# Kernel tuning notes

Hardware: AMD Instinct MI355X
Metric: run time of the kernel (lower is better)

## Reference

```python
import jax, jax.numpy as jnp
import numpy as np

N_NODES = 100000


def setup_inputs() -> dict:
    key = jax.random.key(0)
    ks = jax.random.split(key, 9)
    E = 1600000
    x = jax.random.normal(ks[0], (N_NODES, 12), dtype=jnp.float32)
    edge_index = jax.random.randint(ks[1], (2, E), 0, N_NODES, dtype=jnp.int64)
    def glorot(k, shape):
        lim = float(np.sqrt(6.0 / (shape[0] + shape[1])))
        return jax.random.uniform(k, shape, jnp.float32, -lim, lim)
    return {
        "x": x,
        "edge_index": edge_index,
        "W1": glorot(ks[2], (12, 64)),
        "b1": jnp.zeros((64,), jnp.float32),
        "W2": glorot(ks[3], (64, 128)),
        "b2": jnp.zeros((128,), jnp.float32),
        "W3": glorot(ks[4], (128, 96)),
        "b3": jnp.zeros((96,), jnp.float32),
    }


def reference(x, edge_index, W1, b1, W2, b2, W3, b3):
    N = x.shape[0]
    F_channel, n_his = 8, 12
    src, dst = edge_index[0], edge_index[1]
    # add self loops (PyG GCNConv default)
    loop = jnp.arange(N, dtype=src.dtype)
    src = jnp.concatenate([src, loop])
    dst = jnp.concatenate([dst, loop])
    # symmetric normalization: norm_e = deg[src]^-1/2 * deg[dst]^-1/2
    deg = jax.ops.segment_sum(jnp.ones_like(src, dtype=x.dtype), dst, num_segments=N)
    dinv = jnp.where(deg > 0, jax.lax.rsqrt(deg), 0.0)
    norm = dinv[src] * dinv[dst]  # [E+N]

    def gcn(h, W, b):
        hw = h @ W  # transform first (out_ch <= in-edge fanout cost)
        agg = jax.ops.segment_sum(hw[src] * norm[:, None], dst, num_segments=N)
        return agg + b

    h = jax.nn.relu(gcn(x, W1, b1))
    h = jax.nn.relu(gcn(h, W2, b2))
    h = gcn(h, W3, b3)
    return h.reshape(N, F_channel, n_his)
```

## Files before the change

kernel.cpp:

```cpp
#include <hip/hip_runtime.h>
#include <hip/hip_bf16.h>
#include <hip/hip_fp16.h>


static inline int cdiv(int a, int b) { return (a + b - 1) / b; }
constexpr int BLOCK = 256;
constexpr int BSHIFT = 9;
constexpr int BNODES = 1 << BSHIFT;

typedef float nfloat4 __attribute__((ext_vector_type(4)));
typedef _Float16 f16x8 __attribute__((ext_vector_type(8)));
typedef float f32x16 __attribute__((ext_vector_type(16)));


__device__ __forceinline__ void nt_store_raw16(void* p, float4 v) {
    nfloat4 nv;
    nv.x = v.x; nv.y = v.y; nv.z = v.z; nv.w = v.w;
    __builtin_nontemporal_store(nv, (nfloat4*)p);
}

struct h4 { __half2 a, b; };
__device__ __forceinline__ void store_h4(__half* p, float4 v) {
    h4 r;
    r.a = __floats2half2_rn(v.x, v.y);
    r.b = __floats2half2_rn(v.z, v.w);
    *(h4*)p = r;
}

__device__ __forceinline__ void h8_add(float* acc, float4 raw) {
    union { float4 f; __half2 h[4]; } u;
    u.f = raw;
#pragma unroll
    for (int j = 0; j < 4; ++j) {
        float2 p = __half22float2(u.h[j]);
        acc[2 * j] += p.x;
        acc[2 * j + 1] += p.y;
    }
}


template <int CHUNK>
__global__ void bucket_count_kernel(const int* __restrict__ dst, int E,
                                    int* __restrict__ bcnt, int NB) {
    __shared__ int cnt[256];
    for (int i = threadIdx.x; i < NB; i += blockDim.x) cnt[i] = 0;
    __syncthreads();
    const int e0 = blockIdx.x * CHUNK;
    const int e1 = min(e0 + CHUNK, E);
    for (int e = e0 + threadIdx.x; e < e1; e += blockDim.x)
        atomicAdd(&cnt[dst[e] >> BSHIFT], 1);
    __syncthreads();
    for (int i = threadIdx.x; i < NB; i += blockDim.x)
        if (cnt[i]) atomicAdd(&bcnt[i], cnt[i]);
}

__global__ void bucket_scan_kernel(const int* __restrict__ bcnt, int* __restrict__ gbase,
                                   int* __restrict__ gcur, int NB) {
    __shared__ int tmp[256];
    int t = threadIdx.x;
    int v = (t < NB) ? bcnt[t] : 0;
    tmp[t] = v;
    __syncthreads();
    for (int off = 1; off < 256; off <<= 1) {
        int add = (t >= off) ? tmp[t - off] : 0;
        __syncthreads();
        tmp[t] += add;
        __syncthreads();
    }
    if (t < NB) { int ex = tmp[t] - v; gbase[t] = ex; gcur[t] = ex; }
}

template <int CHUNK>
__global__ void bin_edges_kernel(const int* __restrict__ ei, int E,
                                 int* __restrict__ gcur, unsigned* __restrict__ binned,
                                 int NB) {
    __shared__ int cnt[256], base[256], rk[256];
    for (int i = threadIdx.x; i < NB; i += blockDim.x) { cnt[i] = 0; rk[i] = 0; }
    __syncthreads();
    const int e0 = blockIdx.x * CHUNK;
    const int e1 = min(e0 + CHUNK, E);
    for (int e = e0 + threadIdx.x; e < e1; e += blockDim.x)
        atomicAdd(&cnt[ei[E + e] >> BSHIFT], 1);
    __syncthreads();
    for (int i = threadIdx.x; i < NB; i += blockDim.x)
        base[i] = atomicAdd(&gcur[i], cnt[i]);
    __syncthreads();
    for (int e = e0 + threadIdx.x; e < e1; e += blockDim.x) {
        int s = ei[e], d = ei[E + e];
        int b = d >> BSHIFT;
        int r = atomicAdd(&rk[b], 1);
        binned[base[b] + r] = (unsigned)s | ((unsigned)(d & (BNODES - 1)) << 17);
    }
}

__global__ void csr_fill_kernel(const int* __restrict__ gbase, const int* __restrict__ bcnt,
                                const unsigned* __restrict__ binned,
                                int* __restrict__ deg, float* __restrict__ dinv,
                                int* __restrict__ row_ptr, int* __restrict__ csr_src,
                                int* __restrict__ dh, int N) {
    __shared__ int c[BNODES];
    __shared__ int ps[256];
    __shared__ int dhloc[64];
    const int t = threadIdx.x;
    const int b = blockIdx.x;
    const int node0 = b << BSHIFT;
    if (t < BNODES) c[t] = 0;
    if (t < 64) dhloc[t] = 0;
    __syncthreads();
    const int base = gbase[b];
    const int end = base + bcnt[b];
    for (int e = base + t; e < end; e += 1024)
        atomicAdd(&c[binned[e] >> 17], 1);
    __syncthreads();
    int s0 = 0, s1 = 0;
    if (t < 256) {
        s0 = c[2 * t]; s1 = c[2 * t + 1];
        ps[t] = s0 + s1;
    }
    __syncthreads();
    for (int off = 1; off < 256; off <<= 1) {
        int add = (t >= off && t < 256) ? ps[t - off] : 0;
        __syncthreads();
        if (t < 256) ps[t] += add;
        __syncthreads();
    }
    if (t < 256) {
        const int ex = ps[t] - (s0 + s1);
        const int p0 = base + ex;
        const int p1 = p0 + s0;
        const int n0 = node0 + 2 * t;
        if (n0 < N) {
            row_ptr[n0] = p0; deg[n0] = s0; dinv[n0] = rsqrtf((float)s0 + 1.0f);
            atomicAdd(&dhloc[min(s0, 63)], 1);
            if (n0 + 1 < N) {
                row_ptr[n0 + 1] = p1; deg[n0 + 1] = s1; dinv[n0 + 1] = rsqrtf((float)s1 + 1.0f);
                atomicAdd(&dhloc[min(s1, 63)], 1);
            }
        }
        c[2 * t] = p0; c[2 * t + 1] = p1;
    }
    __syncthreads();
    if (t < 64 && dhloc[t]) atomicAdd(&dh[t], dhloc[t]);
    for (int e = base + t; e < end; e += 1024) {
        unsigned sd = binned[e];
        int pos = atomicAdd(&c[sd >> 17], 1);
        csr_src[pos] = (int)(sd & 0x1FFFFu);
    }
}


__global__ void dscan_kernel(int* __restrict__ dh) {
    __shared__ int tmp[64];
    int t = threadIdx.x;
    int v = dh[t];
    tmp[t] = v;
    __syncthreads();
    for (int off = 1; off < 64; off <<= 1) {
        int add = (t >= off) ? tmp[t - off] : 0;
        __syncthreads();
        tmp[t] += add;
        __syncthreads();
    }
    dh[t] = tmp[t] - v;
}

__global__ void dperm_kernel(const int* __restrict__ deg, const int* __restrict__ row_ptr,
                             const float* __restrict__ dinv, int* __restrict__ dh,
                             int4* __restrict__ hdr, int N) {
    __shared__ int cnt[64], base[64], rk[64];
    const int t = threadIdx.x;
    if (t < 64) { cnt[t] = 0; rk[t] = 0; }
    __syncthreads();
    const int i = blockIdx.x * blockDim.x + t;
    const int d = (i < N) ? deg[i] : 0;
    const int myb = (i < N) ? min(d, 63) : -1;
    if (myb >= 0) atomicAdd(&cnt[myb], 1);
    __syncthreads();
    if (t < 64) base[t] = cnt[t] ? atomicAdd(&dh[t], cnt[t]) : 0;
    __syncthreads();
    if (myb >= 0) {
        int r = atomicAdd(&rk[myb], 1);
        int slot = base[myb] + r;
        int4 h;
        h.x = row_ptr[i];
        h.y = d;
        h.z = i;
        h.w = __float_as_int(dinv[i]);
        hdr[N - 1 - slot] = h;
    }
}


__global__ void prescale_h_kernel(const float* __restrict__ x, const float* __restrict__ dinv,
                                  __half* __restrict__ xs, int N) {
    int i = blockIdx.x * blockDim.x + threadIdx.x;
    if (i >= N) return;
    float di = dinv[i];
    const float4* xr = (const float4*)(x + (size_t)i * 12);
    float4 a = xr[0], b = xr[1], c = xr[2];
    union { float4 f; __half2 h[4]; } u0, u1;
    u0.h[0] = __floats2half2_rn(a.x * di, a.y * di);
    u0.h[1] = __floats2half2_rn(a.z * di, a.w * di);
    u0.h[2] = __floats2half2_rn(b.x * di, b.y * di);
    u0.h[3] = __floats2half2_rn(b.z * di, b.w * di);
    u1.h[0] = __floats2half2_rn(c.x * di, c.y * di);
    u1.h[1] = __floats2half2_rn(c.z * di, c.w * di);
    u1.h[2] = __floats2half2_rn(0.f, 0.f);
    u1.h[3] = __floats2half2_rn(0.f, 0.f);
    float4* op = (float4*)(xs + (size_t)i * 16);
    op[0] = u0.f;
    op[1] = u1.f;
}


__global__ void gather_x_t1_kernel(const int4* __restrict__ hdr,
                                   const int* __restrict__ csr_src,
                                   const __half* __restrict__ xs,
                                   const float* __restrict__ W1,
                                   const float* __restrict__ b1,
                                   __half* __restrict__ h1h, int N) {
    __shared__ float W1s[12 * 64];
    __shared__ float xrow[128][12];
    const int tid = threadIdx.x;
    for (int u = tid; u < 12 * 64 / 4; u += 256)
        ((float4*)W1s)[u] = ((const float4*)W1)[u];

    const int t = blockIdx.x * 256 + tid;
    const bool valid = (t < N * 2);
    const int slot = t >> 1;
    const int c = t & 1;
    const int nl = tid >> 1;
    int4 H = valid ? hdr[slot] : make_int4(0, 0, 0, 0);
    const int* __restrict__ sp = csr_src + H.x;
    const int n = valid ? H.y : 0;
    const int i = H.z;
    const float di = __int_as_float(H.w);
    const int f0 = c * 8;

    float acc[8];
    {
        union { float4 f; __half2 h[4]; } u;
        u.f = *(const float4*)(xs + (size_t)i * 16 + f0);
#pragma unroll
        for (int j = 0; j < 4; ++j) {
            float2 p = __half22float2(u.h[j]);
            acc[2 * j] = p.x; acc[2 * j + 1] = p.y;
        }
    }

    int k = 0;
    if (n >= 8) {
        int s[8];
#pragma unroll
        for (int j = 0; j < 8; ++j) s[j] = sp[j];
        for (; k + 16 <= n; k += 8) {
            int ns[8];
#pragma unroll
            for (int j = 0; j < 8; ++j) ns[j] = sp[k + 8 + j];
            float4 v[8];
#pragma unroll
            for (int j = 0; j < 8; ++j) v[j] = *(const float4*)(xs + (size_t)s[j] * 16 + f0);
#pragma unroll
            for (int j = 0; j < 8; ++j) h8_add(acc, v[j]);
#pragma unroll
            for (int j = 0; j < 8; ++j) s[j] = ns[j];
        }
        float4 v[8];
#pragma unroll
        for (int j = 0; j < 8; ++j) v[j] = *(const float4*)(xs + (size_t)s[j] * 16 + f0);
#pragma unroll
        for (int j = 0; j < 8; ++j) h8_add(acc, v[j]);
        k += 8;
    }
    for (; k + 4 <= n; k += 4) {
        int s0 = sp[k + 0], s1 = sp[k + 1], s2 = sp[k + 2], s3 = sp[k + 3];
        float4 v0 = *(const float4*)(xs + (size_t)s0 * 16 + f0);
        float4 v1 = *(const float4*)(xs + (size_t)s1 * 16 + f0);
        float4 v2 = *(const float4*)(xs + (size_t)s2 * 16 + f0);
        float4 v3 = *(const float4*)(xs + (size_t)s3 * 16 + f0);
        h8_add(acc, v0); h8_add(acc, v1); h8_add(acc, v2); h8_add(acc, v3);
    }
    for (; k < n; ++k) {
        float4 v = *(const float4*)(xs + (size_t)sp[k] * 16 + f0);
        h8_add(acc, v);
    }

    if (valid) {
        if (c == 0) {
#pragma unroll
            for (int j = 0; j < 8; ++j) xrow[nl][j] = acc[j] * di;
        } else {
#pragma unroll
            for (int j = 0; j < 4; ++j) xrow[nl][8 + j] = acc[j] * di;
        }
    }
    __syncthreads();
    if (!valid) return;

    float xr[12];
#pragma unroll
    for (int j = 0; j < 12; ++j) xr[j] = xrow[nl][j];

    __half* op = h1h + (size_t)i * 64 + c * 32;
#pragma unroll
    for (int g = 0; g < 8; ++g) {
        const int c0 = c * 32 + g * 4;
        float4 r = *(const float4*)(b1 + c0);
#pragma unroll
        for (int kk = 0; kk < 12; ++kk) {
            const float4 w = *(const float4*)(W1s + kk * 64 + c0);
            r.x = fmaf(xr[kk], w.x, r.x);
            r.y = fmaf(xr[kk], w.y, r.y);
            r.z = fmaf(xr[kk], w.z, r.z);
            r.w = fmaf(xr[kk], w.w, r.w);
        }
        r.x = fmaxf(r.x, 0.f) * di; r.y = fmaxf(r.y, 0.f) * di;
        r.z = fmaxf(r.z, 0.f) * di; r.w = fmaxf(r.w, 0.f) * di;
        store_h4(op + g * 4, r);
    }
}


__global__ void prep_w_kernel(const float* __restrict__ W2, const float* __restrict__ W3,
                              __half* __restrict__ W2T, __half* __restrict__ W3T) {
    int i = blockIdx.x * 256 + threadIdx.x;
    if (i < 64 * 128) {
        int k = i >> 7, n = i & 127;
        W2T[n * 64 + k] = __float2half(W2[i]);
    } else {
        int j = i - 64 * 128;
        if (j < 128 * 96) {
            int k = j / 96, n = j - k * 96;
            W3T[n * 128 + k] = __float2half(W3[j]);
        }
    }
}

__global__ void __launch_bounds__(256, 2)
fused_g64_t2t3_kernel(const __half* __restrict__ h1h,
                      const int* __restrict__ row_ptr, const int* __restrict__ deg,
                      const int* __restrict__ csr_src, const float* __restrict__ dinv,
                      const __half* __restrict__ W2T,
                      const float* __restrict__ b2,
                      const __half* __restrict__ W3T,
                      __half* __restrict__ out,
                      int N) {
    constexpr int LDH = 136;
    __shared__ _Float16 buf[4][32 * LDH];
    const int tid = threadIdx.x;
    const int lane = tid & 63;
    const int wid = tid >> 6;
    const int l31 = lane & 31;
    const int lh = lane >> 5;
    const int NT = N >> 5;
    const int t0 = blockIdx.x * 4;

    {
        const int nr = tid >> 3;
        const int f0 = (tid & 7) * 8;
#pragma unroll 1
        for (int p = 0; p < 4; ++p) {
            const int t = t0 + p;
            if (t >= NT) break;
            const int i = (t << 5) + nr;
            const int* __restrict__ sp = csr_src + row_ptr[i];
            const int n = deg[i];
            const float di = dinv[i];

            float acc[8];
            {
                union { float4 f; __half2 h[4]; } u;
                u.f = *(const float4*)(h1h + (size_t)i * 64 + f0);
#pragma unroll
                for (int j = 0; j < 4; ++j) {
                    float2 pp = __half22float2(u.h[j]);
                    acc[2 * j] = pp.x; acc[2 * j + 1] = pp.y;
                }
            }

            int k = 0;
            if (n >= 8) {
                int s[8];
#pragma unroll
                for (int j = 0; j < 8; ++j) s[j] = sp[j];
                for (; k + 16 <= n; k += 8) {
                    int ns[8];
#pragma unroll
                    for (int j = 0; j < 8; ++j) ns[j] = sp[k + 8 + j];
                    float4 v[8];
#pragma unroll
                    for (int j = 0; j < 8; ++j) v[j] = *(const float4*)(h1h + (size_t)s[j] * 64 + f0);
#pragma unroll
                    for (int j = 0; j < 8; ++j) h8_add(acc, v[j]);
#pragma unroll
                    for (int j = 0; j < 8; ++j) s[j] = ns[j];
                }
                float4 v[8];
#pragma unroll
                for (int j = 0; j < 8; ++j) v[j] = *(const float4*)(h1h + (size_t)s[j] * 64 + f0);
#pragma unroll
                for (int j = 0; j < 8; ++j) h8_add(acc, v[j]);
                k += 8;
            }
            for (; k + 4 <= n; k += 4) {
                int s0 = sp[k + 0], s1 = sp[k + 1], s2 = sp[k + 2], s3 = sp[k + 3];
                float4 v0 = *(const float4*)(h1h + (size_t)s0 * 64 + f0);
                float4 v1 = *(const float4*)(h1h + (size_t)s1 * 64 + f0);
                float4 v2 = *(const float4*)(h1h + (size_t)s2 * 64 + f0);
                float4 v3 = *(const float4*)(h1h + (size_t)s3 * 64 + f0);
                h8_add(acc, v0); h8_add(acc, v1); h8_add(acc, v2); h8_add(acc, v3);
            }
            for (; k < n; ++k) {
                float4 v = *(const float4*)(h1h + (size_t)sp[k] * 64 + f0);
                h8_add(acc, v);
            }

            union { float4 f; __half2 h[4]; } o;
            o.h[0] = __floats2half2_rn(acc[0] * di, acc[1] * di);
            o.h[1] = __floats2half2_rn(acc[2] * di, acc[3] * di);
            o.h[2] = __floats2half2_rn(acc[4] * di, acc[5] * di);
            o.h[3] = __floats2half2_rn(acc[6] * di, acc[7] * di);
            *(float4*)(&buf[p][nr * LDH + f0]) = o.f;
        }
    }
    __syncthreads();

    const int t = t0 + wid;
    if (t >= NT) return;
    const int r0 = t << 5;
    _Float16* hs = buf[wid];

    float b2v[4];
#pragma unroll
    for (int nt = 0; nt < 4; ++nt) b2v[nt] = b2[nt * 32 + l31];

    f16x8 a2[4];
#pragma unroll
    for (int kb = 0; kb < 4; ++kb)
        a2[kb] = *(const f16x8*)(hs + l31 * LDH + kb * 16 + lh * 8);

#pragma unroll
    for (int nt = 0; nt < 4; ++nt) {
        f32x16 c = {0.f, 0.f, 0.f, 0.f, 0.f, 0.f, 0.f, 0.f,
                    0.f, 0.f, 0.f, 0.f, 0.f, 0.f, 0.f, 0.f};
#pragma unroll
        for (int kb = 0; kb < 4; ++kb) {
            f16x8 b = *(const f16x8*)(W2T + (size_t)(nt * 32 + l31) * 64 + kb * 16 + lh * 8);
            c = __builtin_amdgcn_mfma_f32_32x32x16_f16(a2[kb], b, c, 0, 0, 0);
        }
#pragma unroll
        for (int r = 0; r < 16; ++r) {
            int row = (r & 3) + 8 * (r >> 2) + 4 * lh;
            float v = fmaxf(c[r] + b2v[nt], 0.f);
            hs[row * LDH + nt * 32 + l31] = (_Float16)v;
        }
    }

    f16x8 a3[8];
#pragma unroll
    for (int kb = 0; kb < 8; ++kb)
        a3[kb] = *(const f16x8*)(hs + l31 * LDH + kb * 16 + lh * 8);
    float4 dv[4];
#pragma unroll
    for (int rg = 0; rg < 4; ++rg)
        dv[rg] = *(const float4*)(dinv + r0 + rg * 8 + lh * 4);
#pragma unroll
    for (int nt = 0; nt < 3; ++nt) {
        f32x16 c = {0.f, 0.f, 0.f, 0.f, 0.f, 0.f, 0.f, 0.f,
                    0.f, 0.f, 0.f, 0.f, 0.f, 0.f, 0.f, 0.f};
#pragma unroll
        for (int kb = 0; kb < 8; ++kb) {
            f16x8 b = *(const f16x8*)(W3T + (size_t)(nt * 32 + l31) * 128 + kb * 16 + lh * 8);
            c = __builtin_amdgcn_mfma_f32_32x32x16_f16(a3[kb], b, c, 0, 0, 0);
        }
#pragma unroll
        for (int r = 0; r < 16; ++r) {
            int row = (r & 3) + 8 * (r >> 2) + 4 * lh;
            float dvv = ((const float*)&dv[r >> 2])[r & 3];
            hs[row * LDH + nt * 32 + l31] = (_Float16)(c[r] * dvv);
        }
    }

#pragma unroll
    for (int it = 0; it < 6; ++it) {
        int id = lane + it * 64;
        int row = id / 12, ch = id - row * 12;
        float4 v = *(const float4*)(hs + row * LDH + ch * 8);
        *(float4*)((char*)(out + (size_t)r0 * 96) + (size_t)id * 16) = v;
    }
}


template <int F, bool HAS_BIAS, bool OUT_HALF>
__global__ void gather_h_kernel(const int4* __restrict__ hdr, const int* __restrict__ csr_src,
                                const __half* __restrict__ hws,
                                const float* __restrict__ b, void* __restrict__ out_v, int N) {
    constexpr int TPN = F / 8;
    int t = blockIdx.x * blockDim.x + threadIdx.x;
    if (t >= N * TPN) return;
    int slot = t / TPN;
    int c = t - slot * TPN;
    const int4 H = hdr[slot];
    const int* __restrict__ sp = csr_src + H.x;
    const int n = H.y;
    const int i = H.z;
    const float di = __int_as_float(H.w);
    int f0 = c * 8;

    float acc[8];
    {
        union { float4 f; __half2 h[4]; } u;
        u.f = *(const float4*)(hws + (size_t)i * F + f0);
#pragma unroll
        for (int j = 0; j < 4; ++j) {
            float2 p = __half22float2(u.h[j]);
            acc[2 * j] = p.x; acc[2 * j + 1] = p.y;
        }
    }

    int k = 0;
    if (n >= 8) {
        int s[8];
#pragma unroll
        for (int j = 0; j < 8; ++j) s[j] = sp[j];
        for (; k + 16 <= n; k += 8) {
            int ns[8];
#pragma unroll
            for (int j = 0; j < 8; ++j) ns[j] = sp[k + 8 + j];
            float4 v[8];
#pragma unroll
            for (int j = 0; j < 8; ++j) v[j] = *(const float4*)(hws + (size_t)s[j] * F + f0);
#pragma unroll
            for (int j = 0; j < 8; ++j) h8_add(acc, v[j]);
#pragma unroll
            for (int j = 0; j < 8; ++j) s[j] = ns[j];
        }
        float4 v[8];
#pragma unroll
        for (int j = 0; j < 8; ++j) v[j] = *(const float4*)(hws + (size_t)s[j] * F + f0);
#pragma unroll
        for (int j = 0; j < 8; ++j) h8_add(acc, v[j]);
        k += 8;
    }
    for (; k + 4 <= n; k += 4) {
        int s0 = sp[k + 0], s1 = sp[k + 1], s2 = sp[k + 2], s3 = sp[k + 3];
        float4 v0 = *(const float4*)(hws + (size_t)s0 * F + f0);
        float4 v1 = *(const float4*)(hws + (size_t)s1 * F + f0);
        float4 v2 = *(const float4*)(hws + (size_t)s2 * F + f0);
        float4 v3 = *(const float4*)(hws + (size_t)s3 * F + f0);
        h8_add(acc, v0); h8_add(acc, v1); h8_add(acc, v2); h8_add(acc, v3);
    }
    for (; k < n; ++k) {
        float4 v = *(const float4*)(hws + (size_t)sp[k] * F + f0);
        h8_add(acc, v);
    }

    float4 r0, r1;
    if (HAS_BIAS) {
        const float4 bb0 = *(const float4*)(b + f0);
        const float4 bb1 = *(const float4*)(b + f0 + 4);
        r0.x = fmaf(acc[0], di, bb0.x); r0.y = fmaf(acc[1], di, bb0.y);
        r0.z = fmaf(acc[2], di, bb0.z); r0.w = fmaf(acc[3], di, bb0.w);
        r1.x = fmaf(acc[4], di, bb1.x); r1.y = fmaf(acc[5], di, bb1.y);
        r1.z = fmaf(acc[6], di, bb1.z); r1.w = fmaf(acc[7], di, bb1.w);
    } else {
        r0.x = acc[0] * di; r0.y = acc[1] * di; r0.z = acc[2] * di; r0.w = acc[3] * di;
        r1.x = acc[4] * di; r1.y = acc[5] * di; r1.z = acc[6] * di; r1.w = acc[7] * di;
    }
    if (OUT_HALF) {
        union { float4 f; __half2 h[4]; } u;
        u.h[0] = __floats2half2_rn(r0.x, r0.y);
        u.h[1] = __floats2half2_rn(r0.z, r0.w);
        u.h[2] = __floats2half2_rn(r1.x, r1.y);
        u.h[3] = __floats2half2_rn(r1.z, r1.w);
        nt_store_raw16((__half*)out_v + (size_t)i * F + f0, u.f);
    } else {
        float* op = (float*)out_v + (size_t)i * F + f0;
        nt_store_raw16(op, r0);
        nt_store_raw16(op + 4, r1);
    }
}


extern "C" void kernel_launch(void* const* d_in, const int* in_sizes, int n_in,
                              void* d_out, int out_size, void* d_ws, size_t ws_size,
                              hipStream_t stream) {
    const float* x  = (const float*)d_in[0];
    const int*   ei = (const int*)d_in[1];
    const float* W1 = (const float*)d_in[2];
    const float* b1 = (const float*)d_in[3];
    const float* W2 = (const float*)d_in[4];
    const float* b2 = (const float*)d_in[5];
    const float* W3 = (const float*)d_in[6];
    const float* b3 = (const float*)d_in[7];
    float* out = (float*)d_out;

    const int N = in_sizes[0] / 12;
    const int E = in_sizes[1] / 2;
    const int NB = cdiv(N, BNODES);

    char* ws = (char*)d_ws;
    int*   deg     = (int*)ws;    ws += (size_t)N * sizeof(int);
    int*   row_ptr = (int*)ws;    ws += (size_t)N * sizeof(int);
    int*   bcnt    = (int*)ws;    ws += 256 * sizeof(int);
    int*   dh      = (int*)ws;    ws += 64 * sizeof(int);
    int*   gbase   = (int*)ws;    ws += 256 * sizeof(int);
    int*   gcur    = (int*)ws;    ws += 256 * sizeof(int);
    float* dinv    = (float*)ws;  ws += (size_t)N * sizeof(float);
    int4*  hdr     = (int4*)ws;   ws += (size_t)N * sizeof(int4);
    __half* W2Th   = (__half*)ws; ws += 128 * 64 * sizeof(__half);
    __half* W3Th   = (__half*)ws; ws += 96 * 128 * sizeof(__half);
    int*   csr_src = (int*)ws;    ws += (size_t)E * sizeof(int);
    float* bufA    = (float*)ws;  ws += (size_t)N * 128 * sizeof(float);
    float* bufB    = (float*)ws;
    unsigned* binned = (unsigned*)bufB;

    hipMemsetAsync(bcnt, 0, (256 + 64) * sizeof(int), stream);
    prep_w_kernel<<<80, 256, 0, stream>>>(W2, W3, W2Th, W3Th);
    bucket_count_kernel<8192><<<cdiv(E, 8192), BLOCK, 0, stream>>>(ei + E, E, bcnt, NB);
    bucket_scan_kernel<<<1, 256, 0, stream>>>(bcnt, gbase, gcur, NB);
    bin_edges_kernel<8192><<<cdiv(E, 8192), BLOCK, 0, stream>>>(ei, E, gcur, binned, NB);
    csr_fill_kernel<<<NB, 1024, 0, stream>>>(gbase, bcnt, binned, deg, dinv, row_ptr,
                                             csr_src, dh, N);

    dscan_kernel<<<1, 64, 0, stream>>>(dh);
    dperm_kernel<<<cdiv(N, BLOCK), BLOCK, 0, stream>>>(deg, row_ptr, dinv, dh, hdr, N);

    prescale_h_kernel<<<cdiv(N, BLOCK), BLOCK, 0, stream>>>(x, dinv, (__half*)bufA, N);
    gather_x_t1_kernel<<<cdiv(N * 2, BLOCK), BLOCK, 0, stream>>>(
        hdr, csr_src, (const __half*)bufA, W1, b1, (__half*)bufB, N);

    fused_g64_t2t3_kernel<<<cdiv(N / 32, 4), 256, 0, stream>>>(
        (const __half*)bufB, row_ptr, deg, csr_src, dinv, W2Th, b2, W3Th,
        (__half*)bufA, N);

    gather_h_kernel<96, true, false><<<cdiv(N * 12, BLOCK), BLOCK, 0, stream>>>(
        hdr, csr_src, (const __half*)bufA, b3, out, N);
}
```

Before: 276.2 us.

## Restructure final 96-wide gather into per-block feature slices

The final aggregation kernel used to assign 12 threads per node, each gathering 8 halves. It now launches 8 blocks per group of 256 nodes, and each block handles a 12-feature slice for 256 nodes, one node per thread. Because all threads in a block touch the same 24-byte column slice, the aim is to keep each block's working set smaller and more cache-local, and to cut how many times the index list is re-read per thread group. The cost is narrower 8-byte loads instead of 16-byte ones, more loads per neighbor, and the removal of the 4-way unrolled tail loop.

Measured after the change: 630.6 us. 128% more time.

```diff
diff --git a/kernel.cpp b/kernel.cpp
--- a/kernel.cpp
+++ b/kernel.cpp
@@ -36,6 +36,22 @@
         acc[2 * j] += p.x;
         acc[2 * j + 1] += p.y;
     }
+}
+
+__device__ __forceinline__ void h4_add(float* acc, float2 raw) {
+    union { float2 f; __half2 h[2]; } u;
+    u.f = raw;
+    float2 p0 = __half22float2(u.h[0]);
+    float2 p1 = __half22float2(u.h[1]);
+    acc[0] += p0.x; acc[1] += p0.y; acc[2] += p1.x; acc[3] += p1.y;
+}
+
+__device__ __forceinline__ void h4_set(float* acc, float2 raw) {
+    union { float2 f; __half2 h[2]; } u;
+    u.f = raw;
+    float2 p0 = __half22float2(u.h[0]);
+    float2 p1 = __half22float2(u.h[1]);
+    acc[0] = p0.x; acc[1] = p0.y; acc[2] = p1.x; acc[3] = p1.y;
 }
 
 
@@ -491,31 +507,28 @@
 }
 
 
-template <int F, bool HAS_BIAS, bool OUT_HALF>
-__global__ void gather_h_kernel(const int4* __restrict__ hdr, const int* __restrict__ csr_src,
-                                const __half* __restrict__ hws,
-                                const float* __restrict__ b, void* __restrict__ out_v, int N) {
-    constexpr int TPN = F / 8;
-    int t = blockIdx.x * blockDim.x + threadIdx.x;
-    if (t >= N * TPN) return;
-    int slot = t / TPN;
-    int c = t - slot * TPN;
+__global__ void __launch_bounds__(256)
+gather96_slice_kernel(const int4* __restrict__ hdr, const int* __restrict__ csr_src,
+                      const __half* __restrict__ hws, const float* __restrict__ b,
+                      float* __restrict__ out, int N) {
+    const int bid = blockIdx.x;
+    const int slice = bid & 7;
+    const int slot = (bid >> 3) * 256 + threadIdx.x;
+    if (slot >= N) return;
     const int4 H = hdr[slot];
     const int* __restrict__ sp = csr_src + H.x;
     const int n = H.y;
     const int i = H.z;
     const float di = __int_as_float(H.w);
-    int f0 = c * 8;
-
-    float acc[8];
+    const size_t foff = (size_t)slice * 24;
+    const char* __restrict__ tb = (const char*)hws;
+
+    float acc[12];
     {
-        union { float4 f; __half2 h[4]; } u;
-        u.f = *(const float4*)(hws + (size_t)i * F + f0);
-#pragma unroll
-        for (int j = 0; j < 4; ++j) {
-            float2 p = __half22float2(u.h[j]);
-            acc[2 * j] = p.x; acc[2 * j + 1] = p.y;
-        }
+        const char* rp = tb + (size_t)i * 192 + foff;
+        h4_set(acc + 0, *(const float2*)(rp));
+        h4_set(acc + 4, *(const float2*)(rp + 8));
+        h4_set(acc + 8, *(const float2*)(rp + 16));
     }
 
     int k = 0;
@@ -527,58 +540,46 @@
             int ns[8];
 #pragma unroll
             for (int j = 0; j < 8; ++j) ns[j] = sp[k + 8 + j];
-            float4 v[8];
-#pragma unroll
-            for (int j = 0; j < 8; ++j) v[j] = *(const float4*)(hws + (size_t)s[j] * F + f0);
-#pragma unroll
-            for (int j = 0; j < 8; ++j) h8_add(acc, v[j]);
+#pragma unroll
+            for (int j = 0; j < 8; ++j) {
+                const char* p = tb + (size_t)s[j] * 192 + foff;
+                h4_add(acc + 0, *(const float2*)(p));
+                h4_add(acc + 4, *(const float2*)(p + 8));
+                h4_add(acc + 8, *(const float2*)(p + 16));
+            }
 #pragma unroll
             for (int j = 0; j < 8; ++j) s[j] = ns[j];
         }
-        float4 v[8];
-#pragma unroll
-        for (int j = 0; j < 8; ++j) v[j] = *(const float4*)(hws + (size_t)s[j] * F + f0);
-#pragma unroll
-        for (int j = 0; j < 8; ++j) h8_add(acc, v[j]);
+#pragma unroll
+        for (int j = 0; j < 8; ++j) {
+            const char* p = tb + (size_t)s[j] * 192 + foff;
+            h4_add(acc + 0, *(const float2*)(p));
+            h4_add(acc + 4, *(const float2*)(p + 8));
+            h4_add(acc + 8, *(const float2*)(p + 16));
+        }
         k += 8;
     }
-    for (; k + 4 <= n; k += 4) {
-        int s0 = sp[k + 0], s1 = sp[k + 1], s2 = sp[k + 2], s3 = sp[k + 3];
-        float4 v0 = *(const float4*)(hws + (size_t)s0 * F + f0);
-        float4 v1 = *(const float4*)(hws + (size_t)s1 * F + f0);
-        float4 v2 = *(const float4*)(hws + (size_t)s2 * F + f0);
-        float4 v3 = *(const float4*)(hws + (size_t)s3 * F + f0);
-        h8_add(acc, v0); h8_add(acc, v1); h8_add(acc, v2); h8_add(acc, v3);
-    }
     for (; k < n; ++k) {
-        float4 v = *(const float4*)(hws + (size_t)sp[k] * F + f0);
-        h8_add(acc, v);
-    }
-
-    float4 r0, r1;
-    if (HAS_BIAS) {
-        const float4 bb0 = *(const float4*)(b + f0);
-        const float4 bb1 = *(const float4*)(b + f0 + 4);
-        r0.x = fmaf(acc[0], di, bb0.x); r0.y = fmaf(acc[1], di, bb0.y);
-        r0.z = fmaf(acc[2], di, bb0.z); r0.w = fmaf(acc[3], di, bb0.w);
-        r1.x = fmaf(acc[4], di, bb1.x); r1.y = fmaf(acc[5], di, bb1.y);
-        r1.z = fmaf(acc[6], di, bb1.z); r1.w = fmaf(acc[7], di, bb1.w);
-    } else {
-        r0.x = acc[0] * di; r0.y = acc[1] * di; r0.z = acc[2] * di; r0.w = acc[3] * di;
-        r1.x = acc[4] * di; r1.y = acc[5] * di; r1.z = acc[6] * di; r1.w = acc[7] * di;
-    }
-    if (OUT_HALF) {
-        union { float4 f; __half2 h[4]; } u;
-        u.h[0] = __floats2half2_rn(r0.x, r0.y);
-        u.h[1] = __floats2half2_rn(r0.z, r0.w);
-        u.h[2] = __floats2half2_rn(r1.x, r1.y);
-        u.h[3] = __floats2half2_rn(r1.z, r1.w);
-        nt_store_raw16((__half*)out_v + (size_t)i * F + f0, u.f);
-    } else {
-        float* op = (float*)out_v + (size_t)i * F + f0;
-        nt_store_raw16(op, r0);
-        nt_store_raw16(op + 4, r1);
-    }
+        const char* p = tb + (size_t)sp[k] * 192 + foff;
+        h4_add(acc + 0, *(const float2*)(p));
+        h4_add(acc + 4, *(const float2*)(p + 8));
+        h4_add(acc + 8, *(const float2*)(p + 16));
+    }
+
+    const float4 bb0 = *(const float4*)(b + slice * 12);
+    const float4 bb1 = *(const float4*)(b + slice * 12 + 4);
+    const float4 bb2 = *(const float4*)(b + slice * 12 + 8);
+    float4 r0, r1, r2;
+    r0.x = fmaf(acc[0], di, bb0.x); r0.y = fmaf(acc[1], di, bb0.y);
+    r0.z = fmaf(acc[2], di, bb0.z); r0.w = fmaf(acc[3], di, bb0.w);
+    r1.x = fmaf(acc[4], di, bb1.x); r1.y = fmaf(acc[5], di, bb1.y);
+    r1.z = fmaf(acc[6], di, bb1.z); r1.w = fmaf(acc[7], di, bb1.w);
+    r2.x = fmaf(acc[8], di, bb2.x); r2.y = fmaf(acc[9], di, bb2.y);
+    r2.z = fmaf(acc[10], di, bb2.z); r2.w = fmaf(acc[11], di, bb2.w);
+    float* op = out + (size_t)i * 96 + slice * 12;
+    nt_store_raw16(op, r0);
+    nt_store_raw16(op + 4, r1);
+    nt_store_raw16(op + 8, r2);
 }
 
 
@@ -634,6 +635,6 @@
         (const __half*)bufB, row_ptr, deg, csr_src, dinv, W2Th, b2, W3Th,
         (__half*)bufA, N);
 
-    gather_h_kernel<96, true, false><<<cdiv(N * 12, BLOCK), BLOCK, 0, stream>>>(
+    gather96_slice_kernel<<<cdiv(N, 256) * 8, 256, 0, stream>>>(
         hdr, csr_src, (const __half*)bufA, b3, out, N);
 }
```
